# Performance work log

Hardware: AMD Instinct MI355X
Metric: run time of the kernel (lower is better)

The kernel has to match this reference:

```python
import jax, jax.numpy as jnp
import numpy as np

B, T, D = 2, 2048, 4096
H, G, d = 32, 8, 128
GROUP = H // G  # 4


def setup_inputs() -> dict:
    key = jax.random.key(0)
    ks = jax.random.split(key, 9)
    s = 0.02
    return {
        "hidden_states": jax.random.normal(ks[0], (B, T, D), jnp.float32),
        "Wq": jax.random.normal(ks[1], (D, D), jnp.float32) * s,
        "bq": jax.random.normal(ks[2], (D,), jnp.float32) * s,
        "Wk": jax.random.normal(ks[3], (G * d, D), jnp.float32) * s,
        "bk": jax.random.normal(ks[4], (G * d,), jnp.float32) * s,
        "Wv": jax.random.normal(ks[5], (G * d, D), jnp.float32) * s,
        "bv": jax.random.normal(ks[6], (G * d,), jnp.float32) * s,
        "Wo": jax.random.normal(ks[7], (D, D), jnp.float32) * s,
        "bo": jax.random.normal(ks[8], (D,), jnp.float32) * s,
    }


def reference(hidden_states, Wq, bq, Wk, bk, Wv, bv, Wo, bo):
    # projections (torch Linear: x @ W.T + b)
    q = hidden_states @ Wq.T + bq            # [B,T,D]
    k = hidden_states @ Wk.T + bk            # [B,T,G*d]
    v = hidden_states @ Wv.T + bv            # [B,T,G*d]

    # [B,G,group,T,d] for q; [B,G,T,d] for k,v. repeat_interleave(group, dim=1)
    # on [B,H,...] is exactly the (G, group) grouping of heads.
    q = q.reshape(B, T, G, GROUP, d).transpose(0, 2, 3, 1, 4)  # bgptd
    k = k.reshape(B, T, G, d).transpose(0, 2, 1, 3)            # bgsd
    v = v.reshape(B, T, G, d).transpose(0, 2, 1, 3)            # bgsd

    scale = 1.0 / np.sqrt(d).astype(np.float32)
    scores = jnp.einsum("bgptd,bgsd->bgpts", q, k) * scale     # [B,G,group,Tq,Tk]

    # causal additive mask: (j > i) * -1e9  (past_len = 0)
    i = jnp.arange(T)[:, None]
    j = jnp.arange(T)[None, :]
    causal_add = (j > i).astype(scores.dtype) * -1e9
    scores = scores + causal_add               # broadcast over b,g,p

    attn = jax.nn.softmax(scores, axis=-1)
    y = jnp.einsum("bgpts,bgsd->bgptd", attn, v)               # [B,G,group,T,d]
    y = y.transpose(0, 3, 1, 2, 4).reshape(B, T, D)            # [B,T,H*d]
    return y @ Wo.T + bo
```

## Files before the change

kernel.cpp:

```cpp
#include <hip/hip_runtime.h>
#include <hip/hip_bf16.h>
#include <cstdint>
#include <cstddef>

using bf16 = __hip_bfloat16;
typedef __attribute__((ext_vector_type(8))) short bf16x8;
typedef __attribute__((ext_vector_type(4))) float floatx4;

#define GLOBAL_AS __attribute__((address_space(1)))
#define LDS_AS    __attribute__((address_space(3)))

__device__ __forceinline__ void async_copy16(void* lds, const void* g) {
    __builtin_amdgcn_global_load_lds((GLOBAL_AS void*)(g), (LDS_AS void*)(lds), 16, 0, 0);
}

__device__ __forceinline__ floatx4 mfma_bf16(bf16x8 a, bf16x8 b, floatx4 c) {
    return __builtin_amdgcn_mfma_f32_16x16x32_bf16(a, b, c, 0, 0, 0);
}

__global__ void cvt_f32_bf16(const float* __restrict__ src, bf16* __restrict__ dst, int n) {
    int i = (blockIdx.x * blockDim.x + threadIdx.x) * 4;
    if (i < n) {
        float4 v = *(const float4*)(src + i);
        __align__(8) bf16 t[4];
        t[0] = __float2bfloat16(v.x);
        t[1] = __float2bfloat16(v.y);
        t[2] = __float2bfloat16(v.z);
        t[3] = __float2bfloat16(v.w);
        *(short4*)(dst + i) = *(const short4*)t;
    }
}

template <int OUTF>
__global__ __launch_bounds__(256, 3) void gemm_bt_bias(
    const bf16* __restrict__ A, const bf16* __restrict__ W,
    const float* __restrict__ bias, void* __restrict__ Cv,
    int M, int N, int K, float cscale)
{
    __shared__ __align__(16) bf16 As[128 * 32];
    __shared__ __align__(16) bf16 Ws[128 * 32];

    const int tid  = threadIdx.x;
    const int lane = tid & 63;
    const int wave = tid >> 6;
    const int quad = lane >> 4;
    const int l16  = lane & 15;
    const int wm = (wave >> 1) * 64;
    const int wn = (wave & 1) * 64;

    const int bm = blockIdx.x;
    const int bn = blockIdx.y;

    floatx4 acc[4][4];
#pragma unroll
    for (int i = 0; i < 4; ++i)
#pragma unroll
        for (int j = 0; j < 4; ++j) acc[i][j] = (floatx4){0.f, 0.f, 0.f, 0.f};

    const int srow = tid >> 2;
    const int scol = (tid & 3) * 8;
    const bf16* gA = A + (size_t)(bm * 128 + srow) * K + scol;
    const bf16* gW = W + (size_t)(bn * 128 + srow) * K + scol;
    bf16* lA0 = As + tid * 8;
    bf16* lA1 = As + 2048 + tid * 8;
    bf16* lW0 = Ws + tid * 8;
    bf16* lW1 = Ws + 2048 + tid * 8;
    const size_t skip = (size_t)64 * K;

    const int kt_n = K >> 5;
    for (int kt = 0; kt < kt_n; ++kt) {
        __syncthreads();
        const bf16* ga = gA + kt * 32;
        const bf16* gw = gW + kt * 32;
        async_copy16(lA0, ga);
        async_copy16(lA1, ga + skip);
        async_copy16(lW0, gw);
        async_copy16(lW1, gw + skip);
        __syncthreads();

        bf16x8 af[4], bfr[4];
#pragma unroll
        for (int mi = 0; mi < 4; ++mi)
            af[mi] = *(const bf16x8*)(As + (wm + mi * 16 + l16) * 32 + quad * 8);
#pragma unroll
        for (int ni = 0; ni < 4; ++ni)
            bfr[ni] = *(const bf16x8*)(Ws + (wn + ni * 16 + l16) * 32 + quad * 8);
#pragma unroll
        for (int mi = 0; mi < 4; ++mi)
#pragma unroll
            for (int ni = 0; ni < 4; ++ni)
                acc[mi][ni] = mfma_bf16(af[mi], bfr[ni], acc[mi][ni]);
    }

#pragma unroll
    for (int mi = 0; mi < 4; ++mi) {
        const int row0 = bm * 128 + wm + mi * 16 + quad * 4;
#pragma unroll
        for (int ni = 0; ni < 4; ++ni) {
            const int col = bn * 128 + wn + ni * 16 + l16;
            const float bv = bias[col];
            if (OUTF) {
                float* C = (float*)Cv;
#pragma unroll
                for (int r = 0; r < 4; ++r)
                    C[(size_t)(row0 + r) * N + col] = (acc[mi][ni][r] + bv) * cscale;
            } else {
                bf16* C = (bf16*)Cv;
#pragma unroll
                for (int r = 0; r < 4; ++r)
                    C[(size_t)(row0 + r) * N + col] = __float2bfloat16((acc[mi][ni][r] + bv) * cscale);
            }
        }
    }
}

__global__ __launch_bounds__(256, 3) void gemm_kv(
    const bf16* __restrict__ A,
    const bf16* __restrict__ Wk, const bf16* __restrict__ Wv,
    const float* __restrict__ bk, const float* __restrict__ bv,
    bf16* __restrict__ kout, bf16* __restrict__ vt,
    int M, int K)
{
    __shared__ __align__(16) bf16 As[128 * 32];
    __shared__ __align__(16) bf16 Ws[128 * 32];

    const int tid  = threadIdx.x;
    const int lane = tid & 63;
    const int wave = tid >> 6;
    const int quad = lane >> 4;
    const int l16  = lane & 15;
    const int wm = (wave >> 1) * 64;
    const int wn = (wave & 1) * 64;

    const int bm = blockIdx.x;
    const int bn = blockIdx.y;
    const bool isK = (bn < 8);
    const int nb = isK ? bn : (bn - 8);
    const bf16* Wsel  = isK ? Wk : Wv;
    const float* bsel = isK ? bk : bv;

    floatx4 acc[4][4];
#pragma unroll
    for (int i = 0; i < 4; ++i)
#pragma unroll
        for (int j = 0; j < 4; ++j) acc[i][j] = (floatx4){0.f, 0.f, 0.f, 0.f};

    const int srow = tid >> 2;
    const int scol = (tid & 3) * 8;
    const bf16* gA = A    + (size_t)(bm * 128 + srow) * K + scol;
    const bf16* gW = Wsel + (size_t)(nb * 128 + srow) * K + scol;
    bf16* lA0 = As + tid * 8;
    bf16* lA1 = As + 2048 + tid * 8;
    bf16* lW0 = Ws + tid * 8;
    bf16* lW1 = Ws + 2048 + tid * 8;
    const size_t skip = (size_t)64 * K;

    const int kt_n = K >> 5;
    for (int kt = 0; kt < kt_n; ++kt) {
        __syncthreads();
        const bf16* ga = gA + kt * 32;
        const bf16* gw = gW + kt * 32;
        async_copy16(lA0, ga);
        async_copy16(lA1, ga + skip);
        async_copy16(lW0, gw);
        async_copy16(lW1, gw + skip);
        __syncthreads();

        bf16x8 af[4], bfr[4];
#pragma unroll
        for (int mi = 0; mi < 4; ++mi)
            af[mi] = *(const bf16x8*)(As + (wm + mi * 16 + l16) * 32 + quad * 8);
#pragma unroll
        for (int ni = 0; ni < 4; ++ni)
            bfr[ni] = *(const bf16x8*)(Ws + (wn + ni * 16 + l16) * 32 + quad * 8);
#pragma unroll
        for (int mi = 0; mi < 4; ++mi)
#pragma unroll
            for (int ni = 0; ni < 4; ++ni)
                acc[mi][ni] = mfma_bf16(af[mi], bfr[ni], acc[mi][ni]);
    }

#pragma unroll
    for (int mi = 0; mi < 4; ++mi) {
        const int row0 = bm * 128 + wm + mi * 16 + quad * 4;
#pragma unroll
        for (int ni = 0; ni < 4; ++ni) {
            const int col = nb * 128 + wn + ni * 16 + l16;
            const float bvv = bsel[col];
            if (isK) {
#pragma unroll
                for (int r = 0; r < 4; ++r)
                    kout[(size_t)(row0 + r) * 1024 + col] = __float2bfloat16(acc[mi][ni][r] + bvv);
            } else {
                __align__(8) bf16 tmp[4];
#pragma unroll
                for (int r = 0; r < 4; ++r) tmp[r] = __float2bfloat16(acc[mi][ni][r] + bvv);
                const int b  = row0 >> 11;
                const int t0 = row0 & 2047;
                bf16* dst = vt + ((size_t)(b * 1024 + col)) * 2048 + t0;
                *(short4*)dst = *(const short4*)tmp;
            }
        }
    }
}

__global__ __launch_bounds__(256, 2) void attn_fwd(
    const bf16* __restrict__ qb, const bf16* __restrict__ kb,
    const bf16* __restrict__ vtb, bf16* __restrict__ ob)
{
    constexpr int T  = 2048;
    constexpr int DQ = 4096;
    constexpr int DK = 1024;

    __shared__ __align__(16) bf16 Ks[2][64 * 128];
    __shared__ __align__(16) bf16 Vs[2][128 * 64];
    __shared__ __align__(16) bf16 Ps[4][16][72];

    const int tid  = threadIdx.x;
    const int lane = tid & 63;
    const int wave = tid >> 6;
    const int quad = lane >> 4;
    const int l16  = lane & 15;
    const int swz  = l16 & 7;

    const int qi = blockIdx.x;
    const int bh = blockIdx.y;
    const int b  = bh >> 5;
    const int h  = bh & 31;
    const int g  = h >> 2;
    const int qtB = 31 - qi;
    const int qtA = qi;
    const int q0B = qtB * 64;
    const int q0A = qtA * 64;
    const int qw = wave * 16;

    const bf16* Qg = qb  + (size_t)b * T * DQ + (size_t)h * 128;
    const bf16* Kg = kb  + (size_t)b * T * DK + (size_t)g * 128;
    const bf16* Vg = vtb + ((size_t)b * DK + g * 128) * T;
    bf16*       Og = ob  + (size_t)b * T * DQ + (size_t)h * 128;

    bf16x8 qf[2][4];
    {
        const size_t rB = (size_t)(q0B + qw + l16) * DQ;
        const size_t rA = (size_t)(q0A + qw + l16) * DQ;
#pragma unroll
        for (int kk = 0; kk < 4; ++kk) {
            qf[0][kk] = *(const bf16x8*)(Qg + rB + kk * 32 + quad * 8);
            qf[1][kk] = *(const bf16x8*)(Qg + rA + kk * 32 + quad * 8);
        }
    }

    const int krow_l = tid >> 4;
    const int kc16   = tid & 15;
    const int vrow_l = tid >> 3;
    const int vc16   = tid & 7;

    auto STAGE = [&](int st_, int bi_) {
        const int s0_ = st_ * 64;
        bf16* kbp = &Ks[bi_][0];
        bf16* vbp = &Vs[bi_][0];
#pragma unroll
        for (int i = 0; i < 4; ++i) {
            const int r = i * 16 + krow_l;
            async_copy16(kbp + (i * 256 + tid) * 8,
                         Kg + (size_t)(s0_ + r) * DK + ((kc16 ^ (r & 7)) * 8));
        }
#pragma unroll
        for (int i = 0; i < 4; ++i) {
            const int r = i * 32 + vrow_l;
            async_copy16(vbp + (i * 256 + tid) * 8,
                         Vg + (size_t)r * T + s0_ + ((vc16 ^ (r & 7)) * 8));
        }
    };

    floatx4 oacc[2][8];
#pragma unroll
    for (int t = 0; t < 2; ++t)
#pragma unroll
        for (int i = 0; i < 8; ++i) oacc[t][i] = (floatx4){0.f, 0.f, 0.f, 0.f};
    float m_run[2], l_run[2];
#pragma unroll
    for (int t = 0; t < 2; ++t) { m_run[t] = -1e30f; l_run[t] = 0.f; }

    const int bsrc = (lane & 48) + quad * 4;

    STAGE(0, 0);
    __syncthreads();

    for (int st = 0; st <= qtB; ++st) {
        const int bi = st & 1;
        const int s0 = st * 64;

        if (st < qtB) STAGE(st + 1, bi ^ 1);

        const bf16* Kb = &Ks[bi][0];
        const bf16* Vb = &Vs[bi][0];

        const int ntile = (st <= qtA) ? 2 : 1;
#pragma unroll
        for (int t = 0; t < 2; ++t) {
            if (t >= ntile) break;
            const int q0t  = t ? q0A : q0B;
            const int qt_t = t ? qtA : qtB;

            floatx4 sacc[4];
#pragma unroll
            for (int i = 0; i < 4; ++i) sacc[i] = (floatx4){0.f, 0.f, 0.f, 0.f};
#pragma unroll
            for (int kk = 0; kk < 4; ++kk) {
                const int koff = ((kk * 4 + quad) ^ swz) * 8;
                const bf16x8 qv = qf[t][kk];
#pragma unroll
                for (int ni = 0; ni < 4; ++ni) {
                    bf16x8 kf = *(const bf16x8*)(Kb + (ni * 16 + l16) * 128 + koff);
                    sacc[ni] = mfma_bf16(kf, qv, sacc[ni]);
                }
            }

            const bool diag = (st == qt_t);
            const int qg = q0t + qw + l16;
            float sv[4][4];
#pragma unroll
            for (int ni = 0; ni < 4; ++ni)
#pragma unroll
                for (int r = 0; r < 4; ++r) {
                    float x = sacc[ni][r];
                    if (diag && (s0 + ni * 16 + quad * 4 + r) > qg) x = -1e30f;
                    sv[ni][r] = x;
                }

            float pm[4];
#pragma unroll
            for (int ni = 0; ni < 4; ++ni)
                pm[ni] = fmaxf(fmaxf(sv[ni][0], sv[ni][1]), fmaxf(sv[ni][2], sv[ni][3]));
            float mx = fmaxf(fmaxf(pm[0], pm[1]), fmaxf(pm[2], pm[3]));
            mx = fmaxf(mx, __shfl_xor(mx, 16, 64));
            mx = fmaxf(mx, __shfl_xor(mx, 32, 64));

            const float mold  = m_run[t];
            const float mnew  = fmaxf(mold, mx);
            const float alpha = __expf(mold - mnew);
            m_run[t] = mnew;

            float ssum = 0.f;
#pragma unroll
            for (int ni = 0; ni < 4; ++ni) {
                __align__(8) bf16 pb[4];
#pragma unroll
                for (int r = 0; r < 4; ++r) {
                    float p = __expf(sv[ni][r] - mnew);
                    ssum += p;
                    pb[r] = __float2bfloat16(p);
                }
                *(short4*)&Ps[wave][l16][ni * 16 + quad * 4] = *(const short4*)pb;
            }
            ssum += __shfl_xor(ssum, 16, 64);
            ssum += __shfl_xor(ssum, 32, 64);
            l_run[t] = l_run[t] * alpha + ssum;

            float ar[4];
#pragma unroll
            for (int r = 0; r < 4; ++r) ar[r] = __shfl(alpha, bsrc + r, 64);
#pragma unroll
            for (int db = 0; db < 8; ++db)
#pragma unroll
                for (int r = 0; r < 4; ++r) oacc[t][db][r] *= ar[r];

            asm volatile("s_waitcnt lgkmcnt(0)" ::: "memory");

#pragma unroll
            for (int kk = 0; kk < 2; ++kk) {
                bf16x8 ap = *(const bf16x8*)&Ps[wave][l16][kk * 32 + quad * 8];
                const int voff = ((kk * 4 + quad) ^ swz) * 8;
#pragma unroll
                for (int db = 0; db < 8; ++db) {
                    bf16x8 bv8 = *(const bf16x8*)(Vb + (db * 16 + l16) * 64 + voff);
                    oacc[t][db] = mfma_bf16(ap, bv8, oacc[t][db]);
                }
            }
        }

        __syncthreads();
    }

#pragma unroll
    for (int t = 0; t < 2; ++t) {
        const int q0t = t ? q0A : q0B;
        const float linv = 1.0f / l_run[t];
        float ir[4];
#pragma unroll
        for (int r = 0; r < 4; ++r) ir[r] = __shfl(linv, bsrc + r, 64);
#pragma unroll
        for (int r = 0; r < 4; ++r) {
            const int qg = q0t + qw + quad * 4 + r;
#pragma unroll
            for (int db = 0; db < 8; ++db)
                Og[(size_t)qg * DQ + db * 16 + l16] = __float2bfloat16(oacc[t][db][r] * ir[r]);
        }
    }
}

extern "C" void kernel_launch(void* const* d_in, const int* in_sizes, int n_in,
                              void* d_out, int out_size, void* d_ws, size_t ws_size,
                              hipStream_t stream)
{
    const float* hs = (const float*)d_in[0];
    const float* Wq = (const float*)d_in[1];
    const float* bq = (const float*)d_in[2];
    const float* Wk = (const float*)d_in[3];
    const float* bk = (const float*)d_in[4];
    const float* Wv = (const float*)d_in[5];
    const float* bv = (const float*)d_in[6];
    const float* Wo = (const float*)d_in[7];
    const float* bo = (const float*)d_in[8];
    float* out = (float*)d_out;

    const int M  = 4096;
    const int D  = 4096;
    const int DK = 1024;
    const size_t SZ_D  = (size_t)M * D;
    const size_t SZ_K  = (size_t)M * DK;

    bf16* hsb  = (bf16*)d_ws;
    bf16* Wqb  = hsb  + SZ_D;
    bf16* Wkb  = Wqb  + SZ_D;
    bf16* Wvb  = Wkb  + SZ_K;
    bf16* Wob  = Wvb  + SZ_K;
    bf16* q_buf = Wob + SZ_D;
    bf16* k_buf = q_buf + SZ_D;
    bf16* vt_buf = Wqb;
    bf16* o_buf  = hsb;

    dim3 blk(256);
    const int CB = 256;
    cvt_f32_bf16<<<(int)(SZ_D / 4 + CB - 1) / CB, CB, 0, stream>>>(hs, hsb, (int)SZ_D);
    cvt_f32_bf16<<<(int)(SZ_D / 4 + CB - 1) / CB, CB, 0, stream>>>(Wq, Wqb, (int)SZ_D);
    cvt_f32_bf16<<<(int)(SZ_K / 4 + CB - 1) / CB, CB, 0, stream>>>(Wk, Wkb, (int)SZ_K);
    cvt_f32_bf16<<<(int)(SZ_K / 4 + CB - 1) / CB, CB, 0, stream>>>(Wv, Wvb, (int)SZ_K);
    cvt_f32_bf16<<<(int)(SZ_D / 4 + CB - 1) / CB, CB, 0, stream>>>(Wo, Wob, (int)SZ_D);

    const float scale = 0.08838834764831845f;
    gemm_bt_bias<0><<<dim3(M / 128, D / 128), blk, 0, stream>>>(hsb, Wqb, bq, q_buf, M, D, D, scale);
    gemm_kv<<<dim3(M / 128, 16), blk, 0, stream>>>(hsb, Wkb, Wvb, bk, bv, k_buf, vt_buf, M, D);
    attn_fwd<<<dim3(16, 64), blk, 0, stream>>>(q_buf, k_buf, vt_buf, o_buf);
    gemm_bt_bias<1><<<dim3(M / 128, D / 128), blk, 0, stream>>>(o_buf, Wob, bo, out, M, D, D, 1.0f);
}
```

Baseline: 767.9 us.

## Replace Q and output GEMMs with 256x256 double-buffered swizzled pipelined kernel

The Q-projection and output-projection GEMMs move from 128x128 tiles with K-step 32 and a full sync per step to 256x256 tiles over 8 waves. The new kernel uses K-step 64, XOR-swizzled LDS to avoid bank conflicts, and double-buffered async global-to-LDS loads interleaved with MFMA blocks using setprio and explicit waitcnt. The aim is to raise arithmetic intensity and hide load latency behind matrix math. In exchange, it uses 128KB of LDS per block and a 256-block grid, which lowers occupancy and may leave some CUs idle.

```diff
diff --git a/kernel.cpp b/kernel.cpp
--- a/kernel.cpp
+++ b/kernel.cpp
@@ -31,73 +31,144 @@
     }
 }
 
+#define MMBLK(AF, MB, NB) do {                                                 \
+    __builtin_amdgcn_s_setprio(1);                                             \
+    _Pragma("unroll") for (int kk = 0; kk < 2; ++kk)                           \
+    _Pragma("unroll") for (int mi = 0; mi < 4; ++mi)                           \
+    _Pragma("unroll") for (int ni = 0; ni < 2; ++ni)                           \
+        acc[(MB) + mi][(NB) + ni] =                                            \
+            mfma_bf16(AF[mi][kk], bb[ni][kk], acc[(MB) + mi][(NB) + ni]);      \
+    __builtin_amdgcn_s_setprio(0);                                             \
+} while (0)
+
+#define BAR()   __builtin_amdgcn_s_barrier()
+#define LGKM0() asm volatile("s_waitcnt lgkmcnt(0)" ::: "memory")
+#define VM4()   asm volatile("s_waitcnt vmcnt(4)" ::: "memory")
+#define VM0()   asm volatile("s_waitcnt vmcnt(0)" ::: "memory")
+
 template <int OUTF>
-__global__ __launch_bounds__(256, 3) void gemm_bt_bias(
+__global__ __launch_bounds__(512, 2) void gemm256_bt_bias(
     const bf16* __restrict__ A, const bf16* __restrict__ W,
     const float* __restrict__ bias, void* __restrict__ Cv,
     int M, int N, int K, float cscale)
 {
-    __shared__ __align__(16) bf16 As[128 * 32];
-    __shared__ __align__(16) bf16 Ws[128 * 32];
+    __shared__ __align__(16) bf16 sA[2][2][128 * 64];
+    __shared__ __align__(16) bf16 sB[2][2][128 * 64];
 
     const int tid  = threadIdx.x;
     const int lane = tid & 63;
     const int wave = tid >> 6;
     const int quad = lane >> 4;
     const int l16  = lane & 15;
-    const int wm = (wave >> 1) * 64;
-    const int wn = (wave & 1) * 64;
+    const int wmi  = wave >> 2;
+    const int wni  = wave & 3;
 
     const int bm = blockIdx.x;
     const int bn = blockIdx.y;
 
-    floatx4 acc[4][4];
-#pragma unroll
-    for (int i = 0; i < 4; ++i)
+    const int srow = tid >> 3;
+    const int sc16 = tid & 7;
+
+    auto STAGE = [&](bf16* dst, const bf16* G, int rowbase, int kt) {
+#pragma unroll
+        for (int i = 0; i < 2; ++i) {
+            const int row = i * 64 + srow;
+            async_copy16(dst + (i * 512 + tid) * 8,
+                         G + (size_t)(rowbase + row) * K + kt * 64 + ((sc16 ^ (row & 7)) * 8));
+        }
+    };
+    auto LDA = [&](int bi, int mi, int kk) -> bf16x8 {
+        const bf16* base = &sA[bi][wmi][0];
+        const int r = mi * 16 + l16;
+        return *(const bf16x8*)(base + r * 64 + (((kk * 4 + quad) ^ (r & 7)) * 8));
+    };
+    auto LDB = [&](int bi, int ni, int kk) -> bf16x8 {
+        const bf16* base = &sB[bi][wni >> 1][0];
+        const int r = (wni & 1) * 64 + ni * 16 + l16;
+        return *(const bf16x8*)(base + r * 64 + (((kk * 4 + quad) ^ (r & 7)) * 8));
+    };
+
+    floatx4 acc[8][4];
+#pragma unroll
+    for (int i = 0; i < 8; ++i)
 #pragma unroll
         for (int j = 0; j < 4; ++j) acc[i][j] = (floatx4){0.f, 0.f, 0.f, 0.f};
 
-    const int srow = tid >> 2;
-    const int scol = (tid & 3) * 8;
-    const bf16* gA = A + (size_t)(bm * 128 + srow) * K + scol;
-    const bf16* gW = W + (size_t)(bn * 128 + srow) * K + scol;
-    bf16* lA0 = As + tid * 8;
-    bf16* lA1 = As + 2048 + tid * 8;
-    bf16* lW0 = Ws + tid * 8;
-    bf16* lW1 = Ws + 2048 + tid * 8;
-    const size_t skip = (size_t)64 * K;
-
-    const int kt_n = K >> 5;
-    for (int kt = 0; kt < kt_n; ++kt) {
-        __syncthreads();
-        const bf16* ga = gA + kt * 32;
-        const bf16* gw = gW + kt * 32;
-        async_copy16(lA0, ga);
-        async_copy16(lA1, ga + skip);
-        async_copy16(lW0, gw);
-        async_copy16(lW1, gw + skip);
-        __syncthreads();
-
-        bf16x8 af[4], bfr[4];
-#pragma unroll
-        for (int mi = 0; mi < 4; ++mi)
-            af[mi] = *(const bf16x8*)(As + (wm + mi * 16 + l16) * 32 + quad * 8);
-#pragma unroll
-        for (int ni = 0; ni < 4; ++ni)
-            bfr[ni] = *(const bf16x8*)(Ws + (wn + ni * 16 + l16) * 32 + quad * 8);
-#pragma unroll
-        for (int mi = 0; mi < 4; ++mi)
-#pragma unroll
-            for (int ni = 0; ni < 4; ++ni)
-                acc[mi][ni] = mfma_bf16(af[mi], bfr[ni], acc[mi][ni]);
-    }
-
-#pragma unroll
-    for (int mi = 0; mi < 4; ++mi) {
-        const int row0 = bm * 128 + wm + mi * 16 + quad * 4;
+    const int rowA = bm * 256;
+    const int rowB = bn * 256;
+    const int iters = K >> 7;
+
+    STAGE(&sA[0][0][0], A, rowA + 0,   0);
+    STAGE(&sA[0][1][0], A, rowA + 128, 0);
+    STAGE(&sB[0][0][0], W, rowB + 0,   0);
+    STAGE(&sB[0][1][0], W, rowB + 128, 0);
+    STAGE(&sA[1][0][0], A, rowA + 0,   1);
+    STAGE(&sA[1][1][0], A, rowA + 128, 1);
+    VM4();
+    BAR();
+
+    bf16x8 a0[4][2], a1[4][2], bb[2][2];
+    for (int i = 0; i < iters; ++i) {
+        const int kt = 2 * i;
+        const bool nl = (i + 1 < iters);
+
+#pragma unroll
+        for (int mi = 0; mi < 4; ++mi) { a0[mi][0] = LDA(0, mi, 0); a0[mi][1] = LDA(0, mi, 1); }
+#pragma unroll
+        for (int ni = 0; ni < 2; ++ni) { bb[ni][0] = LDB(0, ni, 0); bb[ni][1] = LDB(0, ni, 1); }
+        STAGE(&sB[1][0][0], W, rowB + 0, kt + 1);
+        BAR(); LGKM0();
+        MMBLK(a0, 0, 0);
+        BAR();
+#pragma unroll
+        for (int mi = 0; mi < 4; ++mi) { a1[mi][0] = LDA(0, mi + 4, 0); a1[mi][1] = LDA(0, mi + 4, 1); }
+        STAGE(&sB[1][1][0], W, rowB + 128, kt + 1);
+        BAR(); LGKM0();
+        MMBLK(a1, 4, 0);
+        BAR();
+#pragma unroll
+        for (int ni = 0; ni < 2; ++ni) { bb[ni][0] = LDB(0, ni + 2, 0); bb[ni][1] = LDB(0, ni + 2, 1); }
+        if (nl) STAGE(&sA[0][0][0], A, rowA + 0, kt + 2);
+        BAR(); LGKM0();
+        MMBLK(a0, 0, 2);
+        BAR();
+        if (nl) { STAGE(&sA[0][1][0], A, rowA + 128, kt + 2); VM4(); }
+        else    { VM0(); }
+        BAR();
+        MMBLK(a1, 4, 2);
+        BAR();
+#pragma unroll
+        for (int mi = 0; mi < 4; ++mi) { a0[mi][0] = LDA(1, mi, 0); a0[mi][1] = LDA(1, mi, 1); }
+#pragma unroll
+        for (int ni = 0; ni < 2; ++ni) { bb[ni][0] = LDB(1, ni, 0); bb[ni][1] = LDB(1, ni, 1); }
+        if (nl) STAGE(&sB[0][0][0], W, rowB + 0, kt + 2);
+        BAR(); LGKM0();
+        MMBLK(a0, 0, 0);
+        BAR();
+#pragma unroll
+        for (int mi = 0; mi < 4; ++mi) { a1[mi][0] = LDA(1, mi + 4, 0); a1[mi][1] = LDA(1, mi + 4, 1); }
+        if (nl) STAGE(&sB[0][1][0], W, rowB + 128, kt + 2);
+        BAR(); LGKM0();
+        MMBLK(a1, 4, 0);
+        BAR();
+#pragma unroll
+        for (int ni = 0; ni < 2; ++ni) { bb[ni][0] = LDB(1, ni + 2, 0); bb[ni][1] = LDB(1, ni + 2, 1); }
+        if (nl) STAGE(&sA[1][0][0], A, rowA + 0, kt + 3);
+        BAR(); LGKM0();
+        MMBLK(a0, 0, 2);
+        BAR();
+        if (nl) { STAGE(&sA[1][1][0], A, rowA + 128, kt + 3); VM4(); }
+        BAR();
+        MMBLK(a1, 4, 2);
+        BAR();
+    }
+
+#pragma unroll
+    for (int mi = 0; mi < 8; ++mi) {
+        const int row0 = bm * 256 + wmi * 128 + mi * 16 + quad * 4;
 #pragma unroll
         for (int ni = 0; ni < 4; ++ni) {
-            const int col = bn * 128 + wn + ni * 16 + l16;
+            const int col = bn * 256 + wni * 64 + ni * 16 + l16;
             const float bv = bias[col];
             if (OUTF) {
                 float* C = (float*)Cv;
@@ -431,7 +502,6 @@
     bf16* vt_buf = Wqb;
     bf16* o_buf  = hsb;
 
-    dim3 blk(256);
     const int CB = 256;
     cvt_f32_bf16<<<(int)(SZ_D / 4 + CB - 1) / CB, CB, 0, stream>>>(hs, hsb, (int)SZ_D);
     cvt_f32_bf16<<<(int)(SZ_D / 4 + CB - 1) / CB, CB, 0, stream>>>(Wq, Wqb, (int)SZ_D);
@@ -440,8 +510,8 @@
     cvt_f32_bf16<<<(int)(SZ_D / 4 + CB - 1) / CB, CB, 0, stream>>>(Wo, Wob, (int)SZ_D);
 
     const float scale = 0.08838834764831845f;
-    gemm_bt_bias<0><<<dim3(M / 128, D / 128), blk, 0, stream>>>(hsb, Wqb, bq, q_buf, M, D, D, scale);
-    gemm_kv<<<dim3(M / 128, 16), blk, 0, stream>>>(hsb, Wkb, Wvb, bk, bv, k_buf, vt_buf, M, D);
-    attn_fwd<<<dim3(16, 64), blk, 0, stream>>>(q_buf, k_buf, vt_buf, o_buf);
-    gemm_bt_bias<1><<<dim3(M / 128, D / 128), blk, 0, stream>>>(o_buf, Wob, bo, out, M, D, D, 1.0f);
-}
+    gemm256_bt_bias<0><<<dim3(M / 256, D / 256), dim3(512), 0, stream>>>(hsb, Wqb, bq, q_buf, M, D, D, scale);
+    gemm_kv<<<dim3(M / 128, 16), dim3(256), 0, stream>>>(hsb, Wkb, Wvb, bk, bv, k_buf, vt_buf, M, D);
+    attn_fwd<<<dim3(16, 64), dim3(256), 0, stream>>>(q_buf, k_buf, vt_buf, o_buf);
+    gemm256_bt_bias<1><<<dim3(M / 256, D / 256), dim3(512), 0, stream>>>(o_buf, Wob, bo, out, M, D, D, 1.0f);
+}
```

After: 746.1 us. 1.03x faster.
